# Kernel optimization log

Measured on AMD Instinct MI355X. Metric: run time of the kernel, lower is better.

Reference implementation:

```python
import jax, jax.numpy as jnp
import numpy as np

THRESH = 0.5
MARGIN = 0.1
SCALE_POS = 2.0
SCALE_NEG = 40.0
EPS = 1e-5


def setup_inputs() -> dict:
    key = jax.random.key(0)
    k1, k2 = jax.random.split(key)
    B, D, C = 8192, 512, 512
    feats = jax.random.normal(k1, (B, D), dtype=jnp.float32)
    labels = jax.random.randint(k2, (B,), 0, C, dtype=jnp.int32)
    return {"feats": feats, "labels": labels}


def reference(feats, labels):
    B = feats.shape[0]
    inv_b = 1.0 / B
    # L2-normalize rows, cosine similarity matrix [B, B]
    f = feats / jnp.linalg.norm(feats, axis=1, keepdims=True)
    sim = f @ f.T

    same = labels[:, None] == labels[None, :]
    # positive pairs: same label AND sim < 1 - eps (excludes self-similarity)
    pos_mask = same & (sim < 1.0 - EPS)
    neg_mask = ~same

    pos_cnt = jnp.sum(pos_mask, axis=1)
    neg_cnt = jnp.sum(neg_mask, axis=1)
    valid1 = (pos_cnt >= 1) & (neg_cnt >= 1)  # row contributes to avg_ap/avg_an

    pos_sum_sim = jnp.sum(jnp.where(pos_mask, sim, 0.0), axis=1)
    neg_sum_sim = jnp.sum(jnp.where(neg_mask, sim, 0.0), axis=1)
    mean_pos = pos_sum_sim / jnp.maximum(pos_cnt, 1)
    mean_neg = neg_sum_sim / jnp.maximum(neg_cnt, 1)

    min_pos = jnp.min(jnp.where(pos_mask, sim, jnp.inf), axis=1)
    max_neg = jnp.max(jnp.where(neg_mask, sim, -jnp.inf), axis=1)

    # hard mining: neg_pair + margin > min(pos), pos_pair - margin < max(neg)
    neg_sel = neg_mask & (sim + MARGIN > min_pos[:, None])
    pos_sel = pos_mask & (sim - MARGIN < max_neg[:, None])
    valid2 = (jnp.sum(pos_sel, axis=1) >= 1) & (jnp.sum(neg_sel, axis=1) >= 1)
    valid = valid1 & valid2

    pos_exp = jnp.sum(jnp.where(pos_sel, jnp.exp(-SCALE_POS * (sim - THRESH)), 0.0), axis=1)
    neg_exp = jnp.sum(jnp.where(neg_sel, jnp.exp(SCALE_NEG * (sim - THRESH)), 0.0), axis=1)
    row_loss = (1.0 / SCALE_POS) * jnp.log1p(pos_exp) + (1.0 / SCALE_NEG) * jnp.log1p(neg_exp)

    loss = jnp.sum(jnp.where(valid, row_loss, 0.0)) * inv_b
    avg_ap = jnp.sum(jnp.where(valid1, mean_pos, 0.0)) * inv_b
    avg_an = jnp.sum(jnp.where(valid1, mean_neg, 0.0)) * inv_b
    return (loss.reshape(-1), avg_ap, avg_an)
```

## Files before the change

### kernel.cpp

```cpp
#include <hip/hip_runtime.h>
#include <math.h>

typedef float floatx4 __attribute__((ext_vector_type(4)));
typedef short short8 __attribute__((ext_vector_type(8)));
typedef unsigned short ushort4v __attribute__((ext_vector_type(4)));
typedef unsigned short ushort8v __attribute__((ext_vector_type(8)));
typedef unsigned int uint4v __attribute__((ext_vector_type(4)));

#define MARGIN_ 0.1f
#define THRESH_ 0.5f
#define LOG2E_ 1.44269504088896f

__device__ __forceinline__ unsigned short f2bf(float f){
  unsigned int x = __float_as_uint(f);
  x += 0x7FFFu + ((x >> 16) & 1u);
  return (unsigned short)(x >> 16);
}
__device__ __forceinline__ float bf2f(unsigned short u){
  return __uint_as_float(((unsigned int)u) << 16);
}

__device__ __forceinline__ void gld16(const unsigned short* g, unsigned short* l){
  __builtin_amdgcn_global_load_lds(
      (const __attribute__((address_space(1))) unsigned int*)(g),
      (__attribute__((address_space(3))) unsigned int*)(l), 16, 0, 0);
}

__global__ __launch_bounds__(64) void k_norm(const float* __restrict__ feats,
                                             unsigned short* __restrict__ fbf){
  const int row = blockIdx.x;
  const int l = threadIdx.x;
  const float* rp = feats + (size_t)row * 512;
  float4 v0 = ((const float4*)rp)[2 * l];
  float4 v1 = ((const float4*)rp)[2 * l + 1];
  float ss = v0.x*v0.x + v0.y*v0.y + v0.z*v0.z + v0.w*v0.w
           + v1.x*v1.x + v1.y*v1.y + v1.z*v1.z + v1.w*v1.w;
  #pragma unroll
  for(int m = 1; m < 64; m <<= 1) ss += __shfl_xor(ss, m);
  const float rn = 1.0f / sqrtf(ss);
  short8 pk;
  pk[0] = (short)f2bf(v0.x*rn); pk[1] = (short)f2bf(v0.y*rn);
  pk[2] = (short)f2bf(v0.z*rn); pk[3] = (short)f2bf(v0.w*rn);
  pk[4] = (short)f2bf(v1.x*rn); pk[5] = (short)f2bf(v1.y*rn);
  pk[6] = (short)f2bf(v1.z*rn); pk[7] = (short)f2bf(v1.w*rn);
  ((short8*)(fbf + (size_t)row * 512))[l] = pk;
}

__global__ __launch_bounds__(256) void k_prep(const int* __restrict__ labels,
                                              unsigned short* __restrict__ labp,
                                              int* __restrict__ cnt, int Bn){
  const int i = blockIdx.x * 256 + threadIdx.x;
  if(i < Bn){
    labp[i] = (unsigned short)labels[(i & ~63) + ((i & 3) * 16) + ((i >> 2) & 15)];
    atomicAdd(&cnt[labels[i]], 1);
  }
}

#define TRI_S(y) ((y)*n - (((y)*((y)-1))>>1))
__global__ __launch_bounds__(256) void k_gemm_sym(const unsigned short* __restrict__ fbf,
                                                  unsigned short* __restrict__ simb,
                                                  int Bn, int nTri){
  const int n = Bn >> 7;
  int i = blockIdx.x;
  int j;
  if((nTri & 7) == 0){ const int c = nTri >> 3; j = (i & 7) * c + (i >> 3); }
  else j = i;
  int by = (int)(((float)(2*n + 1) - sqrtf((float)((2*n+1)*(2*n+1) - 8*j))) * 0.5f);
  if(by < 0) by = 0;
  while(TRI_S(by + 1) <= j) by++;
  while(TRI_S(by) > j) by--;
  const int bx = by + (j - TRI_S(by));
  const bool diag = (by == bx);

  __shared__ __align__(16) unsigned short Ald[128 * 32];
  __shared__ __align__(16) unsigned short Bld[128 * 32];

  const int t = threadIdx.x;
  const int lane = t & 63, wave = t >> 6;
  const int wm = wave >> 1, wn = wave & 1;
  const int lc = lane & 15, lk = lane >> 4;
  const int row0 = by * 128, col0 = bx * 128;

  floatx4 acc[4][4];
  #pragma unroll
  for(int a = 0; a < 4; a++)
    #pragma unroll
    for(int b2 = 0; b2 < 4; b2++) acc[a][b2] = (floatx4){0.f, 0.f, 0.f, 0.f};

  const int rsub  = lane >> 2;
  const int slotg = (lane & 3) ^ ((lane >> 3) & 3);
  const unsigned short* gA0 = fbf + (size_t)(row0 + wave*32 + rsub) * 512 + slotg * 8;
  const unsigned short* gB0 = fbf + (size_t)(col0 + wave*32 + rsub) * 512 + slotg * 8;
  unsigned short* lA0 = Ald + wave * 1024;
  unsigned short* lB0 = Bld + wave * 1024;
  const int kswz = lk ^ ((lc >> 1) & 3);

  for(int k0 = 0; k0 < 512; k0 += 32){
    __syncthreads();
    gld16(gA0 + k0,            lA0);
    gld16(gA0 + 16*512 + k0,   lA0 + 512);
    gld16(gB0 + k0,            lB0);
    gld16(gB0 + 16*512 + k0,   lB0 + 512);
    __syncthreads();
    short8 av[4], bv[4];
    #pragma unroll
    for(int mi = 0; mi < 4; mi++) av[mi] = ((const short8*)Ald)[(wm*64 + mi*16 + lc)*4 + kswz];
    #pragma unroll
    for(int ni = 0; ni < 4; ni++) bv[ni] = ((const short8*)Bld)[(wn*64 + ni*16 + lc)*4 + kswz];
    #pragma unroll
    for(int mi = 0; mi < 4; mi++)
      #pragma unroll
      for(int ni = 0; ni < 4; ni++)
        acc[mi][ni] = __builtin_amdgcn_mfma_f32_16x16x32_bf16(av[mi], bv[ni], acc[mi][ni], 0, 0, 0);
  }

  unsigned short b[4][4][4];
  #pragma unroll
  for(int mi = 0; mi < 4; mi++)
    #pragma unroll
    for(int ni = 0; ni < 4; ni++)
      #pragma unroll
      for(int r = 0; r < 4; r++) b[mi][ni][r] = f2bf(acc[mi][ni][r]);

  #pragma unroll
  for(int mi = 0; mi < 4; mi++){
    #pragma unroll
    for(int r = 0; r < 4; r++){
      const int row = row0 + wm*64 + mi*16 + lk*4 + r;
      ushort4v v;
      v[0] = b[mi][0][r]; v[1] = b[mi][1][r]; v[2] = b[mi][2][r]; v[3] = b[mi][3][r];
      *(ushort4v*)(simb + (size_t)row * Bn + col0 + wn*64 + lc*4) = v;
    }
  }

  if(!diag){
    #pragma unroll
    for(int ni = 0; ni < 4; ni++){
      const size_t crow = (size_t)(col0 + wn*64 + ni*16 + lc) * Bn;
      #pragma unroll
      for(int h = 0; h < 2; h++){
        ushort8v v;
        v[0] = b[0][ni][2*h];   v[1] = b[1][ni][2*h];
        v[2] = b[2][ni][2*h];   v[3] = b[3][ni][2*h];
        v[4] = b[0][ni][2*h+1]; v[5] = b[1][ni][2*h+1];
        v[6] = b[2][ni][2*h+1]; v[7] = b[3][ni][2*h+1];
        *(ushort8v*)(simb + crow + row0 + wm*64 + 16*lk + 8*h) = v;
      }
    }
  }
}

template<int NPT>
__global__ __launch_bounds__(256) void k_fused(const unsigned short* __restrict__ simb,
                                               const int* __restrict__ labels,
                                               const unsigned short* __restrict__ labp,
                                               const int* __restrict__ cnt,
                                               float* __restrict__ rl,
                                               float* __restrict__ apv,
                                               float* __restrict__ anv, int Bn){
  const int row = blockIdx.x;
  const int t = threadIdx.x, lane = t & 63, wave = t >> 6;
  const unsigned short* srow = simb + (size_t)row * Bn;
  const int labi = labels[row];
  const int a = row & 63;
  const int selfpos = (row & ~63) + ((a & 15) * 4) + (a >> 4);

  __shared__ float rq0[4], rq1[4], rq2[4], rq3[4];

  uint4v sv[NPT];
  unsigned int pmask[NPT], nmask[NPT];

  float ps = 0.f, tot = 0.f, mn = INFINITY, mx = -INFINITY;
  #pragma unroll
  for(int c = 0; c < NPT; c++){
    const int idx = c * 256 + t;
    sv[c] = ((const uint4v*)srow)[idx];
    const uint4v lb = ((const uint4v*)labp)[idx];
    const int j0 = idx * 8;
    const int so = selfpos - j0;
    const unsigned int selfm = ((unsigned int)so < 8u) ? (1u << so) : 0u;
    unsigned int sm = 0;
    #pragma unroll
    for(int k = 0; k < 4; k++){
      const unsigned int lw = lb[k];
      sm |= (((int)(lw & 0xFFFFu) == labi) ? 1u : 0u) << (2*k);
      sm |= (((int)(lw >> 16)     == labi) ? 1u : 0u) << (2*k + 1);
    }
    const unsigned int pm = sm & ~selfm;
    pmask[c] = pm;
    nmask[c] = (~sm) & 0xFFu;
    #pragma unroll
    for(int k = 0; k < 4; k++){
      const unsigned int w = sv[c][k];
      const float slo = __uint_as_float(w << 16);
      const float shi = __uint_as_float(w & 0xFFFF0000u);
      tot += slo + shi;
      const bool plo = (pm >> (2*k)) & 1u,  phi = (pm >> (2*k+1)) & 1u;
      const bool nlo = (nmask[c] >> (2*k)) & 1u, nhi = (nmask[c] >> (2*k+1)) & 1u;
      ps += plo ? slo : 0.f;  ps += phi ? shi : 0.f;
      mn = plo ? fminf(mn, slo) : mn;  mn = phi ? fminf(mn, shi) : mn;
      mx = nlo ? fmaxf(mx, slo) : mx;  mx = nhi ? fmaxf(mx, shi) : mx;
    }
    if(selfm){
      const unsigned int w = sv[c][so >> 1];
      tot -= (so & 1) ? __uint_as_float(w & 0xFFFF0000u) : __uint_as_float(w << 16);
    }
  }
  #pragma unroll
  for(int m = 1; m < 64; m <<= 1){
    ps += __shfl_xor(ps, m); tot += __shfl_xor(tot, m);
    mn = fminf(mn, __shfl_xor(mn, m)); mx = fmaxf(mx, __shfl_xor(mx, m));
  }
  if(lane == 0){ rq0[wave] = ps; rq1[wave] = tot; rq2[wave] = mn; rq3[wave] = mx; }
  __syncthreads();
  const float bps    = rq0[0] + rq0[1] + rq0[2] + rq0[3];
  const float btot   = rq1[0] + rq1[1] + rq1[2] + rq1[3];
  const float minpos = fminf(fminf(rq2[0], rq2[1]), fminf(rq2[2], rq2[3]));
  const float maxneg = fmaxf(fmaxf(rq3[0], rq3[1]), fmaxf(rq3[2], rq3[3]));

  const float KP1 = -2.0f * LOG2E_, KP0 = 1.0f * LOG2E_;
  const float KN1 = 40.0f * LOG2E_, KN0 = -20.0f * LOG2E_;
  float pe = 0.f, ne = 0.f;
  #pragma unroll
  for(int c = 0; c < NPT; c++){
    const unsigned int pm = pmask[c], nm = nmask[c];
    #pragma unroll
    for(int k = 0; k < 4; k++){
      const unsigned int w = sv[c][k];
      #pragma unroll
      for(int h = 0; h < 2; h++){
        const float s = h ? __uint_as_float(w & 0xFFFF0000u)
                          : __uint_as_float(w << 16);
        const int e = 2*k + h;
        const bool isp = (pm >> e) & 1u;
        const bool isn = (nm >> e) & 1u;
        const float ex = exp2f(fmaf(s, isp ? KP1 : KN1, isp ? KP0 : KN0));
        const bool psel = isp && (s - MARGIN_ < maxneg);
        const bool nsel = isn && (s + MARGIN_ > minpos);
        pe += psel ? ex : 0.f;
        ne += nsel ? ex : 0.f;
      }
    }
  }
  #pragma unroll
  for(int m = 1; m < 64; m <<= 1){
    pe += __shfl_xor(pe, m); ne += __shfl_xor(ne, m);
  }
  if(lane == 0){ rq0[wave] = pe; rq1[wave] = ne; }
  __syncthreads();
  if(t == 0){
    const float spe = rq0[0] + rq0[1] + rq0[2] + rq0[3];
    const float sne = rq1[0] + rq1[1] + rq1[2] + rq1[3];
    const int c = cnt[labi];
    const float pc = (float)(c - 1);
    const float nc = (float)(Bn - c);
    const bool v1 = (pc >= 1.f) && (nc >= 1.f);
    const bool pf = (minpos - MARGIN_ < maxneg);
    const bool nf = (maxneg + MARGIN_ > minpos);
    const bool valid = v1 && pf && nf;
    rl[row]  = valid ? (0.5f * log1pf(spe) + 0.025f * log1pf(sne)) : 0.f;
    apv[row] = v1 ? bps / fmaxf(pc, 1.f) : 0.f;
    anv[row] = v1 ? (btot - bps) / fmaxf(nc, 1.f) : 0.f;
  }
}

__global__ __launch_bounds__(256) void k_fused_gen(const unsigned short* __restrict__ simb,
                                                   const int* __restrict__ labels,
                                                   const unsigned short* __restrict__ labp,
                                                   const int* __restrict__ cnt,
                                                   float* __restrict__ rl,
                                                   float* __restrict__ apv,
                                                   float* __restrict__ anv, int Bn){
  const int row = blockIdx.x;
  const int t = threadIdx.x, lane = t & 63, wave = t >> 6;
  const unsigned short* srow = simb + (size_t)row * Bn;
  const int labi = labels[row];
  const int a = row & 63;
  const int selfpos = (row & ~63) + ((a & 15) * 4) + (a >> 4);
  const int npt = Bn >> 11;

  __shared__ float rq0[4], rq1[4], rq2[4], rq3[4];

  float ps = 0.f, tot = 0.f, mn = INFINITY, mx = -INFINITY;
  for(int c2 = 0; c2 < npt; c2++){
    const int idx = c2 * 256 + t;
    const ushort8v svv = ((const ushort8v*)srow)[idx];
    const ushort8v lb = ((const ushort8v*)labp)[idx];
    const int j0 = idx * 8;
    #pragma unroll
    for(int e = 0; e < 8; e++){
      const float s = bf2f(svv[e]);
      const bool same = ((int)lb[e] == labi);
      const bool self = ((j0 + e) == selfpos);
      if(!self) tot += s;
      if(same && !self){ ps += s; mn = fminf(mn, s); }
      if(!same) mx = fmaxf(mx, s);
    }
  }
  #pragma unroll
  for(int m = 1; m < 64; m <<= 1){
    ps += __shfl_xor(ps, m); tot += __shfl_xor(tot, m);
    mn = fminf(mn, __shfl_xor(mn, m)); mx = fmaxf(mx, __shfl_xor(mx, m));
  }
  if(lane == 0){ rq0[wave] = ps; rq1[wave] = tot; rq2[wave] = mn; rq3[wave] = mx; }
  __syncthreads();
  const float bps    = rq0[0] + rq0[1] + rq0[2] + rq0[3];
  const float btot   = rq1[0] + rq1[1] + rq1[2] + rq1[3];
  const float minpos = fminf(fminf(rq2[0], rq2[1]), fminf(rq2[2], rq2[3]));
  const float maxneg = fmaxf(fmaxf(rq3[0], rq3[1]), fmaxf(rq3[2], rq3[3]));

  float pe = 0.f, ne = 0.f;
  for(int c2 = 0; c2 < npt; c2++){
    const int idx = c2 * 256 + t;
    const ushort8v svv = ((const ushort8v*)srow)[idx];
    const ushort8v lb = ((const ushort8v*)labp)[idx];
    const int j0 = idx * 8;
    #pragma unroll
    for(int e = 0; e < 8; e++){
      const float s = bf2f(svv[e]);
      const bool same = ((int)lb[e] == labi);
      const bool self = ((j0 + e) == selfpos);
      const bool psel = same && !self && (s - MARGIN_ < maxneg);
      const bool nsel = (!same) && (s + MARGIN_ > minpos);
      const float ex = exp2f(fmaf(s, psel ? (-2.0f*LOG2E_) : (40.0f*LOG2E_),
                                     psel ? LOG2E_ : (-20.0f*LOG2E_)));
      pe += psel ? ex : 0.f;
      ne += nsel ? ex : 0.f;
    }
  }
  #pragma unroll
  for(int m = 1; m < 64; m <<= 1){
    pe += __shfl_xor(pe, m); ne += __shfl_xor(ne, m);
  }
  if(lane == 0){ rq0[wave] = pe; rq1[wave] = ne; }
  __syncthreads();
  if(t == 0){
    const float spe = rq0[0] + rq0[1] + rq0[2] + rq0[3];
    const float sne = rq1[0] + rq1[1] + rq1[2] + rq1[3];
    const int c = cnt[labi];
    const float pc = (float)(c - 1);
    const float nc = (float)(Bn - c);
    const bool v1 = (pc >= 1.f) && (nc >= 1.f);
    const bool pf = (minpos - MARGIN_ < maxneg);
    const bool nf = (maxneg + MARGIN_ > minpos);
    const bool valid = v1 && pf && nf;
    rl[row]  = valid ? (0.5f * log1pf(spe) + 0.025f * log1pf(sne)) : 0.f;
    apv[row] = v1 ? bps / fmaxf(pc, 1.f) : 0.f;
    anv[row] = v1 ? (btot - bps) / fmaxf(nc, 1.f) : 0.f;
  }
}

__global__ __launch_bounds__(256) void k_sum(const float* __restrict__ rl,
                                             const float* __restrict__ apv,
                                             const float* __restrict__ anv,
                                             float* __restrict__ blk, int Bn){
  const int t = threadIdx.x;
  const int row = blockIdx.x * 256 + t;
  float r = rl[row], a1 = apv[row], a2 = anv[row];
  #pragma unroll
  for(int off = 32; off; off >>= 1){
    r += __shfl_down(r, off); a1 += __shfl_down(a1, off); a2 += __shfl_down(a2, off);
  }
  __shared__ float red[3][4];
  const int lane = t & 63, wave = t >> 6;
  if(lane == 0){ red[0][wave] = r; red[1][wave] = a1; red[2][wave] = a2; }
  __syncthreads();
  if(t == 0){
    blk[blockIdx.x*3 + 0] = red[0][0] + red[0][1] + red[0][2] + red[0][3];
    blk[blockIdx.x*3 + 1] = red[1][0] + red[1][1] + red[1][2] + red[1][3];
    blk[blockIdx.x*3 + 2] = red[2][0] + red[2][1] + red[2][2] + red[2][3];
  }
}

__global__ void k_final(const float* __restrict__ blk, int nblk, float inv_b,
                        float* __restrict__ out){
  if(threadIdx.x == 0 && blockIdx.x == 0){
    float l = 0, a = 0, n = 0;
    for(int i = 0; i < nblk; i++){ l += blk[i*3]; a += blk[i*3 + 1]; n += blk[i*3 + 2]; }
    out[0] = l * inv_b;
    out[1] = a * inv_b;
    out[2] = n * inv_b;
  }
}

__global__ __launch_bounds__(256) void k_pass1(const unsigned short* __restrict__ fbf,
                                               const int* __restrict__ labels,
                                               float* __restrict__ part,
                                               int Bn, int ncb){
  __shared__ __align__(16) unsigned short Ald[128 * 32];
  __shared__ __align__(16) unsigned short Bld[128 * 32];
  __shared__ int Lrow[128], Lcol[128];
  __shared__ float Sps[2][128], Stot[2][128], Smin[2][128], Smax[2][128];

  const int t = threadIdx.x;
  const int lane = t & 63, wave = t >> 6;
  const int wm = wave >> 1, wn = wave & 1;
  const int lc = lane & 15, lk = lane >> 4;
  const int row0 = blockIdx.y * 128, col0 = blockIdx.x * 128;

  if(t < 128){
    Lrow[t] = labels[row0 + t];
    Lcol[t] = labels[col0 + t];
  }

  floatx4 acc[4][4];
  #pragma unroll
  for(int i = 0; i < 4; i++)
    #pragma unroll
    for(int j = 0; j < 4; j++) acc[i][j] = (floatx4){0.f, 0.f, 0.f, 0.f};

  const int rsub  = lane >> 2;
  const int slotg = (lane & 3) ^ ((lane >> 3) & 3);
  const unsigned short* gA0 = fbf + (size_t)(row0 + wave*32 + rsub) * 512 + slotg * 8;
  const unsigned short* gB0 = fbf + (size_t)(col0 + wave*32 + rsub) * 512 + slotg * 8;
  unsigned short* lA0 = Ald + wave * 1024;
  unsigned short* lB0 = Bld + wave * 1024;
  const int kswz = lk ^ ((lc >> 1) & 3);

  for(int k0 = 0; k0 < 512; k0 += 32){
    __syncthreads();
    gld16(gA0 + k0,            lA0);
    gld16(gA0 + 16*512 + k0,   lA0 + 512);
    gld16(gB0 + k0,            lB0);
    gld16(gB0 + 16*512 + k0,   lB0 + 512);
    __syncthreads();
    short8 av[4], bv[4];
    #pragma unroll
    for(int mi = 0; mi < 4; mi++) av[mi] = ((const short8*)Ald)[(wm*64 + mi*16 + lc)*4 + kswz];
    #pragma unroll
    for(int ni = 0; ni < 4; ni++) bv[ni] = ((const short8*)Bld)[(wn*64 + ni*16 + lc)*4 + kswz];
    #pragma unroll
    for(int mi = 0; mi < 4; mi++)
      #pragma unroll
      for(int ni = 0; ni < 4; ni++)
        acc[mi][ni] = __builtin_amdgcn_mfma_f32_16x16x32_bf16(av[mi], bv[ni], acc[mi][ni], 0, 0, 0);
  }

  int labj[4], gj[4];
  #pragma unroll
  for(int ni = 0; ni < 4; ni++){
    const int cl = wn*64 + ni*16 + lc;
    labj[ni] = Lcol[cl]; gj[ni] = col0 + cl;
  }
  #pragma unroll
  for(int mi = 0; mi < 4; mi++){
    #pragma unroll
    for(int r = 0; r < 4; r++){
      const int rowl = wm*64 + mi*16 + lk*4 + r;
      const int labi = Lrow[rowl];
      const int gi = row0 + rowl;
      float ps = 0.f, tot = 0.f, mn = INFINITY, mx = -INFINITY;
      #pragma unroll
      for(int ni = 0; ni < 4; ni++){
        const float s = acc[mi][ni][r];
        const bool same = (labi == labj[ni]);
        const bool self = (gi == gj[ni]);
        if(!self) tot += s;
        if(same && !self){ ps += s; mn = fminf(mn, s); }
        if(!same) mx = fmaxf(mx, s);
      }
      #pragma unroll
      for(int m = 1; m < 16; m <<= 1){
        ps += __shfl_xor(ps, m); tot += __shfl_xor(tot, m);
        mn = fminf(mn, __shfl_xor(mn, m)); mx = fmaxf(mx, __shfl_xor(mx, m));
      }
      if(lc == 0){
        Sps[wn][rowl] = ps; Stot[wn][rowl] = tot;
        Smin[wn][rowl] = mn; Smax[wn][rowl] = mx;
      }
    }
  }
  __syncthreads();
  if(t < 128){
    const size_t stride = (size_t)ncb * Bn;
    const size_t base = (size_t)blockIdx.x * Bn + row0 + t;
    part[0*stride + base] = Sps[0][t] + Sps[1][t];
    part[1*stride + base] = Stot[0][t] + Stot[1][t];
    part[2*stride + base] = fminf(Smin[0][t], Smin[1][t]);
    part[3*stride + base] = fmaxf(Smax[0][t], Smax[1][t]);
  }
}

__global__ __launch_bounds__(256) void k_reduce1(const float* __restrict__ part,
                                                 const int* __restrict__ labels,
                                                 const int* __restrict__ cnt,
                                                 float* __restrict__ st,
                                                 int Bn, int ncb){
  const int row = blockIdx.x * 256 + threadIdx.x;
  if(row >= Bn) return;
  const size_t stride = (size_t)ncb * Bn;
  float ps = 0, tot = 0, mn = INFINITY, mx = -INFINITY;
  for(int cb = 0; cb < ncb; cb++){
    const size_t base = (size_t)cb * Bn + row;
    ps  += part[0*stride + base];
    tot += part[1*stride + base];
    mn = fminf(mn, part[2*stride + base]);
    mx = fmaxf(mx, part[3*stride + base]);
  }
  const int c = cnt[labels[row]];
  const float pc = (float)(c - 1);
  const float nc = (float)(Bn - c);
  st[0*Bn + row] = mn;
  st[1*Bn + row] = mx;
  st[2*Bn + row] = ps / fmaxf(pc, 1.f);
  st[3*Bn + row] = (tot - ps) / fmaxf(nc, 1.f);
  st[4*Bn + row] = (pc >= 1.f && nc >= 1.f) ? 1.f : 0.f;
}

__global__ __launch_bounds__(256) void k_pass2(const unsigned short* __restrict__ fbf,
                                               const int* __restrict__ labels,
                                               const float* __restrict__ st,
                                               float* __restrict__ part,
                                               int Bn, int ncb){
  __shared__ __align__(16) unsigned short Ald[128 * 32];
  __shared__ __align__(16) unsigned short Bld[128 * 32];
  __shared__ int Lrow[128], Lcol[128];
  __shared__ float Minp[128], Maxn[128];
  __shared__ float Spe[2][128], Sne[2][128], Spf[2][128], Snf[2][128];

  const int t = threadIdx.x;
  const int lane = t & 63, wave = t >> 6;
  const int wm = wave >> 1, wn = wave & 1;
  const int lc = lane & 15, lk = lane >> 4;
  const int row0 = blockIdx.y * 128, col0 = blockIdx.x * 128;

  if(t < 128){
    Lrow[t] = labels[row0 + t];
    Lcol[t] = labels[col0 + t];
    Minp[t] = st[0*Bn + row0 + t];
    Maxn[t] = st[1*Bn + row0 + t];
  }

  floatx4 acc[4][4];
  #pragma unroll
  for(int i = 0; i < 4; i++)
    #pragma unroll
    for(int j = 0; j < 4; j++) acc[i][j] = (floatx4){0.f, 0.f, 0.f, 0.f};

  const int rsub  = lane >> 2;
  const int slotg = (lane & 3) ^ ((lane >> 3) & 3);
  const unsigned short* gA0 = fbf + (size_t)(row0 + wave*32 + rsub) * 512 + slotg * 8;
  const unsigned short* gB0 = fbf + (size_t)(col0 + wave*32 + rsub) * 512 + slotg * 8;
  unsigned short* lA0 = Ald + wave * 1024;
  unsigned short* lB0 = Bld + wave * 1024;
  const int kswz = lk ^ ((lc >> 1) & 3);

  for(int k0 = 0; k0 < 512; k0 += 32){
    __syncthreads();
    gld16(gA0 + k0,            lA0);
    gld16(gA0 + 16*512 + k0,   lA0 + 512);
    gld16(gB0 + k0,            lB0);
    gld16(gB0 + 16*512 + k0,   lB0 + 512);
    __syncthreads();
    short8 av[4], bv[4];
    #pragma unroll
    for(int mi = 0; mi < 4; mi++) av[mi] = ((const short8*)Ald)[(wm*64 + mi*16 + lc)*4 + kswz];
    #pragma unroll
    for(int ni = 0; ni < 4; ni++) bv[ni] = ((const short8*)Bld)[(wn*64 + ni*16 + lc)*4 + kswz];
    #pragma unroll
    for(int mi = 0; mi < 4; mi++)
      #pragma unroll
      for(int ni = 0; ni < 4; ni++)
        acc[mi][ni] = __builtin_amdgcn_mfma_f32_16x16x32_bf16(av[mi], bv[ni], acc[mi][ni], 0, 0, 0);
  }

  int labj[4], gj[4];
  #pragma unroll
  for(int ni = 0; ni < 4; ni++){
    const int cl = wn*64 + ni*16 + lc;
    labj[ni] = Lcol[cl]; gj[ni] = col0 + cl;
  }
  #pragma unroll
  for(int mi = 0; mi < 4; mi++){
    #pragma unroll
    for(int r = 0; r < 4; r++){
      const int rowl = wm*64 + mi*16 + lk*4 + r;
      const int labi = Lrow[rowl];
      const int gi = row0 + rowl;
      const float mp  = Minp[rowl];
      const float mxn = Maxn[rowl];
      float pe = 0.f, ne = 0.f;
      bool pa = false, na = false;
      #pragma unroll
      for(int ni = 0; ni < 4; ni++){
        const float s = acc[mi][ni][r];
        const bool same = (labi == labj[ni]);
        const bool self = (gi == gj[ni]);
        if(same && !self && (s - MARGIN_ < mxn)){
          pe += __expf(-2.0f * (s - THRESH_)); pa = true;
        }
        if(!same && (s + MARGIN_ > mp)){
          ne += __expf(40.0f * (s - THRESH_)); na = true;
        }
      }
      const unsigned long long bp  = __ballot((int)pa);
      const unsigned long long bn2 = __ballot((int)na);
      #pragma unroll
      for(int m = 1; m < 16; m <<= 1){
        pe += __shfl_xor(pe, m); ne += __shfl_xor(ne, m);
      }
      if(lc == 0){
        Spe[wn][rowl] = pe; Sne[wn][rowl] = ne;
        Spf[wn][rowl] = ((bp  >> (lk*16)) & 0xFFFFull) ? 1.f : 0.f;
        Snf[wn][rowl] = ((bn2 >> (lk*16)) & 0xFFFFull) ? 1.f : 0.f;
      }
    }
  }
  __syncthreads();
  if(t < 128){
    const size_t stride = (size_t)ncb * Bn;
    const size_t base = (size_t)blockIdx.x * Bn + row0 + t;
    part[0*stride + base] = Spe[0][t] + Spe[1][t];
    part[1*stride + base] = Sne[0][t] + Sne[1][t];
    part[2*stride + base] = fmaxf(Spf[0][t], Spf[1][t]);
    part[3*stride + base] = fmaxf(Snf[0][t], Snf[1][t]);
  }
}

__global__ __launch_bounds__(256) void k_reduce2f(const float* __restrict__ part,
                                                  const float* __restrict__ st,
                                                  float* __restrict__ rowloss,
                                                  float* __restrict__ apv,
                                                  float* __restrict__ anv,
                                                  int Bn, int ncb){
  const int row = blockIdx.x * 256 + threadIdx.x;
  if(row >= Bn) return;
  const size_t stride = (size_t)ncb * Bn;
  float pe = 0, ne = 0, pf = 0, nf = 0;
  for(int cb = 0; cb < ncb; cb++){
    const size_t base = (size_t)cb * Bn + row;
    pe += part[0*stride + base]; ne += part[1*stride + base];
    pf = fmaxf(pf, part[2*stride + base]); nf = fmaxf(nf, part[3*stride + base]);
  }
  const float v1 = st[4*Bn + row];
  const bool valid = (v1 > 0.5f) && (pf > 0.5f) && (nf > 0.5f);
  rowloss[row] = valid ? (0.5f * log1pf(pe) + 0.025f * log1pf(ne)) : 0.f;
  apv[row] = (v1 > 0.5f) ? st[2*Bn + row] : 0.f;
  anv[row] = (v1 > 0.5f) ? st[3*Bn + row] : 0.f;
}

extern "C" void kernel_launch(void* const* d_in, const int* in_sizes, int n_in,
                              void* d_out, int out_size, void* d_ws, size_t ws_size,
                              hipStream_t stream){
  const float* feats = (const float*)d_in[0];
  const int* labels = (const int*)d_in[1];
  float* out = (float*)d_out;
  const int Bn  = in_sizes[1];
  const int ncb = Bn / 128;
  const int nTri = ncb * (ncb + 1) / 2;

  char* ws = (char*)d_ws;
  size_t off = 0;
  unsigned short* fbf = (unsigned short*)(ws + off); off += (size_t)Bn * 512 * 2;
  float* part = (float*)(ws + off); off += (size_t)4 * ncb * Bn * 4;
  float* st   = (float*)(ws + off); off += (size_t)5 * Bn * 4;
  int*   cnt  = (int*)(ws + off);   off += 4096;
  unsigned short* labp = (unsigned short*)(ws + off); off += (size_t)Bn * 2;
  off = (off + 255) & ~(size_t)255;
  float* rl   = (float*)(ws + off); off += (size_t)Bn * 4;
  float* apv  = (float*)(ws + off); off += (size_t)Bn * 4;
  float* anv  = (float*)(ws + off); off += (size_t)Bn * 4;
  float* blk  = (float*)(ws + off); off += 4096;
  off = (off + 255) & ~(size_t)255;
  unsigned short* simb = (unsigned short*)(ws + off);
  const size_t need = off + (size_t)Bn * Bn * 2;
  const bool mat = (ws_size >= need);

  (void)hipMemsetAsync(cnt, 0, 512 * sizeof(int), stream);
  k_norm<<<Bn, 64, 0, stream>>>(feats, fbf);
  k_prep<<<(Bn + 255) / 256, 256, 0, stream>>>(labels, labp, cnt, Bn);
  if(mat){
    k_gemm_sym<<<nTri, 256, 0, stream>>>(fbf, simb, Bn, nTri);
    if(Bn == 8192){
      k_fused<4><<<Bn, 256, 0, stream>>>(simb, labels, labp, cnt, rl, apv, anv, Bn);
    } else {
      k_fused_gen<<<Bn, 256, 0, stream>>>(simb, labels, labp, cnt, rl, apv, anv, Bn);
    }
  } else {
    dim3 g(ncb, Bn / 128);
    k_pass1<<<g, 256, 0, stream>>>(fbf, labels, part, Bn, ncb);
    k_reduce1<<<Bn / 256, 256, 0, stream>>>(part, labels, cnt, st, Bn, ncb);
    k_pass2<<<g, 256, 0, stream>>>(fbf, labels, st, part, Bn, ncb);
    k_reduce2f<<<Bn / 256, 256, 0, stream>>>(part, st, rl, apv, anv, Bn, ncb);
  }
  k_sum<<<Bn / 256, 256, 0, stream>>>(rl, apv, anv, blk, Bn);
  k_final<<<1, 64, 0, stream>>>(blk, Bn / 256, 1.0f / (float)Bn, out);
}
```

Baseline: 153.5 us.

## Compute positive and total similarity sums via class centroid dot products

Builds per-class member lists in the label prep kernel and adds two small kernels that form class centroid sums and a global feature sum. The fused row kernel then gets the positive and total similarity sums as dot products of the row's features with these vectors, minus a self term, instead of accumulating them over the similarity matrix. Self-exclusion masks are dropped from the min/max pass, and the hard-mining thresholds are precomputed. In exchange it adds two launches, one of which serializes 512 loads per thread over only two blocks. It also caps class membership at 48, and the sums now come from bf16 features rather than bf16 similarities, which changes rounding.

```diff
diff --git a/kernel.cpp b/kernel.cpp
--- a/kernel.cpp
+++ b/kernel.cpp
@@ -10,6 +10,7 @@
 #define MARGIN_ 0.1f
 #define THRESH_ 0.5f
 #define LOG2E_ 1.44269504088896f
+#define MCAP 48
 
 __device__ __forceinline__ unsigned short f2bf(float f){
   unsigned int x = __float_as_uint(f);
@@ -48,12 +49,41 @@
 
 __global__ __launch_bounds__(256) void k_prep(const int* __restrict__ labels,
                                               unsigned short* __restrict__ labp,
-                                              int* __restrict__ cnt, int Bn){
+                                              int* __restrict__ cnt,
+                                              int* __restrict__ members, int Bn){
   const int i = blockIdx.x * 256 + threadIdx.x;
   if(i < Bn){
     labp[i] = (unsigned short)labels[(i & ~63) + ((i & 3) * 16) + ((i >> 2) & 15)];
-    atomicAdd(&cnt[labels[i]], 1);
-  }
+    const int l = labels[i];
+    const int pos = atomicAdd(&cnt[l], 1);
+    if(pos < MCAP) members[l * MCAP + pos] = i;
+  }
+}
+
+__global__ __launch_bounds__(256) void k_cent(const unsigned short* __restrict__ fbf,
+                                              const int* __restrict__ members,
+                                              const int* __restrict__ cnt,
+                                              float* __restrict__ C){
+  const int c = blockIdx.x;
+  const int t = threadIdx.x;
+  const int m = min(cnt[c], MCAP);
+  float a0 = 0.f, a1 = 0.f;
+  for(int k = 0; k < m; k++){
+    const int j = members[c * MCAP + k];
+    const unsigned int w = *(const unsigned int*)(fbf + (size_t)j * 512 + 2 * t);
+    a0 += __uint_as_float(w << 16);
+    a1 += __uint_as_float(w & 0xFFFF0000u);
+  }
+  C[(size_t)c * 512 + 2*t]     = a0;
+  C[(size_t)c * 512 + 2*t + 1] = a1;
+}
+
+__global__ __launch_bounds__(256) void k_s(const float* __restrict__ C,
+                                           float* __restrict__ S){
+  const int d = blockIdx.x * 256 + threadIdx.x;
+  float a = 0.f;
+  for(int c = 0; c < 512; c++) a += C[(size_t)c * 512 + d];
+  S[d] = a;
 }
 
 #define TRI_S(y) ((y)*n - (((y)*((y)-1))>>1))
@@ -152,8 +182,11 @@
 
 template<int NPT>
 __global__ __launch_bounds__(256) void k_fused(const unsigned short* __restrict__ simb,
+                                               const unsigned short* __restrict__ fbf,
                                                const int* __restrict__ labels,
                                                const unsigned short* __restrict__ labp,
+                                               const float* __restrict__ C,
+                                               const float* __restrict__ S,
                                                const int* __restrict__ cnt,
                                                float* __restrict__ rl,
                                                float* __restrict__ apv,
@@ -162,81 +195,72 @@
   const int t = threadIdx.x, lane = t & 63, wave = t >> 6;
   const unsigned short* srow = simb + (size_t)row * Bn;
   const int labi = labels[row];
-  const int a = row & 63;
-  const int selfpos = (row & ~63) + ((a & 15) * 4) + (a >> 4);
-
-  __shared__ float rq0[4], rq1[4], rq2[4], rq3[4];
-
-  uint4v sv[NPT];
-  unsigned int pmask[NPT], nmask[NPT];
-
-  float ps = 0.f, tot = 0.f, mn = INFINITY, mx = -INFINITY;
+
+  __shared__ float rq0[4], rq1[4], rq2[4], rq3[4], rq4[4];
+
+  const unsigned int wf = *(const unsigned int*)(fbf + (size_t)row * 512 + 2*t);
+  const float f0 = __uint_as_float(wf << 16);
+  const float f1 = __uint_as_float(wf & 0xFFFF0000u);
+  const float2 cv = *(const float2*)(C + (size_t)labi * 512 + 2*t);
+  const float2 s2 = *(const float2*)(S + 2*t);
+  float dps   = f0*cv.x + f1*cv.y;
+  float dtot  = f0*s2.x + f1*s2.y;
+  float dself = f0*f0 + f1*f1;
+
+  uint4v sv[NPT], lb[NPT];
+  float mn = INFINITY, mx = -INFINITY;
   #pragma unroll
   for(int c = 0; c < NPT; c++){
     const int idx = c * 256 + t;
     sv[c] = ((const uint4v*)srow)[idx];
-    const uint4v lb = ((const uint4v*)labp)[idx];
-    const int j0 = idx * 8;
-    const int so = selfpos - j0;
-    const unsigned int selfm = ((unsigned int)so < 8u) ? (1u << so) : 0u;
-    unsigned int sm = 0;
-    #pragma unroll
-    for(int k = 0; k < 4; k++){
-      const unsigned int lw = lb[k];
-      sm |= (((int)(lw & 0xFFFFu) == labi) ? 1u : 0u) << (2*k);
-      sm |= (((int)(lw >> 16)     == labi) ? 1u : 0u) << (2*k + 1);
-    }
-    const unsigned int pm = sm & ~selfm;
-    pmask[c] = pm;
-    nmask[c] = (~sm) & 0xFFu;
+    lb[c] = ((const uint4v*)labp)[idx];
     #pragma unroll
     for(int k = 0; k < 4; k++){
       const unsigned int w = sv[c][k];
+      const unsigned int lw = lb[c][k];
       const float slo = __uint_as_float(w << 16);
       const float shi = __uint_as_float(w & 0xFFFF0000u);
-      tot += slo + shi;
-      const bool plo = (pm >> (2*k)) & 1u,  phi = (pm >> (2*k+1)) & 1u;
-      const bool nlo = (nmask[c] >> (2*k)) & 1u, nhi = (nmask[c] >> (2*k+1)) & 1u;
-      ps += plo ? slo : 0.f;  ps += phi ? shi : 0.f;
-      mn = plo ? fminf(mn, slo) : mn;  mn = phi ? fminf(mn, shi) : mn;
-      mx = nlo ? fmaxf(mx, slo) : mx;  mx = nhi ? fmaxf(mx, shi) : mx;
-    }
-    if(selfm){
-      const unsigned int w = sv[c][so >> 1];
-      tot -= (so & 1) ? __uint_as_float(w & 0xFFFF0000u) : __uint_as_float(w << 16);
+      const bool smlo = ((int)(lw & 0xFFFFu) == labi);
+      const bool smhi = ((int)(lw >> 16)     == labi);
+      mn = fminf(mn, smlo ? slo :  INFINITY);
+      mn = fminf(mn, smhi ? shi :  INFINITY);
+      mx = fmaxf(mx, smlo ? -INFINITY : slo);
+      mx = fmaxf(mx, smhi ? -INFINITY : shi);
     }
   }
   #pragma unroll
   for(int m = 1; m < 64; m <<= 1){
-    ps += __shfl_xor(ps, m); tot += __shfl_xor(tot, m);
+    dps += __shfl_xor(dps, m); dtot += __shfl_xor(dtot, m); dself += __shfl_xor(dself, m);
     mn = fminf(mn, __shfl_xor(mn, m)); mx = fmaxf(mx, __shfl_xor(mx, m));
   }
-  if(lane == 0){ rq0[wave] = ps; rq1[wave] = tot; rq2[wave] = mn; rq3[wave] = mx; }
-  __syncthreads();
-  const float bps    = rq0[0] + rq0[1] + rq0[2] + rq0[3];
-  const float btot   = rq1[0] + rq1[1] + rq1[2] + rq1[3];
+  if(lane == 0){ rq0[wave] = dps; rq1[wave] = dtot; rq2[wave] = mn; rq3[wave] = mx; rq4[wave] = dself; }
+  __syncthreads();
+  const float sdself = rq4[0] + rq4[1] + rq4[2] + rq4[3];
+  const float bps    = (rq0[0] + rq0[1] + rq0[2] + rq0[3]) - sdself;
+  const float btot   = (rq1[0] + rq1[1] + rq1[2] + rq1[3]) - sdself;
   const float minpos = fminf(fminf(rq2[0], rq2[1]), fminf(rq2[2], rq2[3]));
   const float maxneg = fmaxf(fmaxf(rq3[0], rq3[1]), fmaxf(rq3[2], rq3[3]));
+  __syncthreads();
 
   const float KP1 = -2.0f * LOG2E_, KP0 = 1.0f * LOG2E_;
   const float KN1 = 40.0f * LOG2E_, KN0 = -20.0f * LOG2E_;
+  const float TP = maxneg + MARGIN_;
+  const float TN = minpos - MARGIN_;
   float pe = 0.f, ne = 0.f;
   #pragma unroll
   for(int c = 0; c < NPT; c++){
-    const unsigned int pm = pmask[c], nm = nmask[c];
     #pragma unroll
     for(int k = 0; k < 4; k++){
       const unsigned int w = sv[c][k];
+      const unsigned int lw = lb[c][k];
       #pragma unroll
       for(int h = 0; h < 2; h++){
         const float s = h ? __uint_as_float(w & 0xFFFF0000u)
                           : __uint_as_float(w << 16);
-        const int e = 2*k + h;
-        const bool isp = (pm >> e) & 1u;
-        const bool isn = (nm >> e) & 1u;
-        const float ex = exp2f(fmaf(s, isp ? KP1 : KN1, isp ? KP0 : KN0));
-        const bool psel = isp && (s - MARGIN_ < maxneg);
-        const bool nsel = isn && (s + MARGIN_ > minpos);
+        const bool same = ((int)(h ? (lw >> 16) : (lw & 0xFFFFu)) == labi);
+        const float ex = exp2f(fmaf(s, same ? KP1 : KN1, same ? KP0 : KN0));
+        const bool psel = same && (s < TP);
+        const bool nsel = (!same) && (s > TN);
         pe += psel ? ex : 0.f;
         ne += nsel ? ex : 0.f;
       }
@@ -308,7 +332,10 @@
   const float btot   = rq1[0] + rq1[1] + rq1[2] + rq1[3];
   const float minpos = fminf(fminf(rq2[0], rq2[1]), fminf(rq2[2], rq2[3]));
   const float maxneg = fmaxf(fmaxf(rq3[0], rq3[1]), fmaxf(rq3[2], rq3[3]));
-
+  __syncthreads();
+
+  const float TP = maxneg + MARGIN_;
+  const float TN = minpos - MARGIN_;
   float pe = 0.f, ne = 0.f;
   for(int c2 = 0; c2 < npt; c2++){
     const int idx = c2 * 256 + t;
@@ -320,8 +347,8 @@
       const float s = bf2f(svv[e]);
       const bool same = ((int)lb[e] == labi);
       const bool self = ((j0 + e) == selfpos);
-      const bool psel = same && !self && (s - MARGIN_ < maxneg);
-      const bool nsel = (!same) && (s + MARGIN_ > minpos);
+      const bool psel = same && !self && (s < TP);
+      const bool nsel = (!same) && (s > TN);
       const float ex = exp2f(fmaf(s, psel ? (-2.0f*LOG2E_) : (40.0f*LOG2E_),
                                      psel ? LOG2E_ : (-20.0f*LOG2E_)));
       pe += psel ? ex : 0.f;
@@ -657,6 +684,9 @@
   int*   cnt  = (int*)(ws + off);   off += 4096;
   unsigned short* labp = (unsigned short*)(ws + off); off += (size_t)Bn * 2;
   off = (off + 255) & ~(size_t)255;
+  int*   members = (int*)(ws + off); off += (size_t)512 * MCAP * 4;
+  float* Cc  = (float*)(ws + off);  off += (size_t)512 * 512 * 4;
+  float* Sv  = (float*)(ws + off);  off += 512 * 4;
   float* rl   = (float*)(ws + off); off += (size_t)Bn * 4;
   float* apv  = (float*)(ws + off); off += (size_t)Bn * 4;
   float* anv  = (float*)(ws + off); off += (size_t)Bn * 4;
@@ -668,11 +698,15 @@
 
   (void)hipMemsetAsync(cnt, 0, 512 * sizeof(int), stream);
   k_norm<<<Bn, 64, 0, stream>>>(feats, fbf);
-  k_prep<<<(Bn + 255) / 256, 256, 0, stream>>>(labels, labp, cnt, Bn);
+  k_prep<<<(Bn + 255) / 256, 256, 0, stream>>>(labels, labp, cnt, members, Bn);
   if(mat){
+    if(Bn == 8192){
+      k_cent<<<512, 256, 0, stream>>>(fbf, members, cnt, Cc);
+      k_s<<<2, 256, 0, stream>>>(Cc, Sv);
+    }
     k_gemm_sym<<<nTri, 256, 0, stream>>>(fbf, simb, Bn, nTri);
     if(Bn == 8192){
-      k_fused<4><<<Bn, 256, 0, stream>>>(simb, labels, labp, cnt, rl, apv, anv, Bn);
+      k_fused<4><<<Bn, 256, 0, stream>>>(simb, fbf, labels, labp, Cc, Sv, cnt, rl, apv, anv, Bn);
     } else {
       k_fused_gen<<<Bn, 256, 0, stream>>>(simb, labels, labp, cnt, rl, apv, anv, Bn);
     }
```

Result: slower. 160.4 us (+4.5%).
